# Optimization experiments

Measured on AMD Instinct MI355X. Metric: run time of the kernel, lower is better.

The kernel has to match this reference:

```python
import jax, jax.numpy as jnp
import numpy as np

VOC = 32000; D = 512; DFF = 2048; L = 4; H = 8; DH = D // H
NN = 256; K = 8; NB = 32; R = 128; SMAX = 1024; B = 4; S = 1024
STD = 0.02


def _ln(x, s, b):
    m = x.mean(-1, keepdims=True)
    v = ((x - m) ** 2).mean(-1, keepdims=True)
    return (x - m) / jnp.sqrt(v + 1e-5) * s + b


def setup_inputs() -> dict:
    key = jax.random.key(0)
    ks = jax.random.split(key, 24)
    p = {}
    p["input_ids"] = jax.random.randint(ks[0], (B, S), 0, VOC)
    p["token_emb"] = jax.random.normal(ks[1], (VOC, D)) * STD
    p["pos_emb"] = jax.random.normal(ks[2], (SMAX, D)) * STD
    # fixed shared basis buffers (orthogonalized at init in torch; random stand-in, same forward math)
    bA = jax.random.normal(ks[3], (NB, D, R))
    p["basis_A"] = bA / jnp.linalg.norm(bA.reshape(NB, -1), axis=-1)[:, None, None]
    be = jax.random.normal(ks[4], (NB, D))
    p["basis_emb"] = be / jnp.linalg.norm(be, axis=-1, keepdims=True)
    # per-layer params stacked on leading L axis; torch Linear weight is [out, in]
    p["q_w"] = jax.random.normal(ks[5], (L, D, D)) * STD
    p["q_b"] = jnp.zeros((L, D))
    p["k_w"] = jax.random.normal(ks[6], (L, D, D)) * STD
    p["k_b"] = jnp.zeros((L, D))
    p["ao_w"] = jax.random.normal(ks[7], (L, D, D)) * STD
    p["ao_b"] = jnp.zeros((L, D))
    p["recipe"] = jax.random.normal(ks[8], (L, NN, NB)) * 0.5
    p["ctx_pat"] = jax.random.normal(ks[9], (L, NN, H)) * 0.5
    p["vout_w"] = jax.random.normal(ks[10], (L, D, R)) * STD
    p["vout_b"] = jnp.zeros((L, D))
    p["up_w"] = jax.random.normal(ks[11], (L, DFF, D)) * STD
    p["up_b"] = jnp.zeros((L, DFF))
    p["down_w"] = jax.random.normal(ks[12], (L, D, DFF)) * STD
    p["down_b"] = jnp.zeros((L, D))
    p["ln1_s"] = jnp.ones((L, D)); p["ln1_b"] = jnp.zeros((L, D))
    p["ln2_s"] = jnp.ones((L, D)); p["ln2_b"] = jnp.zeros((L, D))
    p["lnf_s"] = jnp.ones((D,)); p["lnf_b"] = jnp.zeros((D,))
    return p


def reference(input_ids, token_emb, pos_emb, basis_A, basis_emb,
              q_w, q_b, k_w, k_b, ao_w, ao_b, recipe, ctx_pat,
              vout_w, vout_b, up_w, up_b, down_w, down_b,
              ln1_s, ln1_b, ln2_s, ln2_b, lnf_s, lnf_b):
    Bb, Ss = input_ids.shape
    x = token_emb[input_ids] + pos_emb[:Ss][None]  # [B,S,D]
    causal = jnp.tril(jnp.ones((Ss, Ss), dtype=bool))
    scale = 1.0 / np.sqrt(DH)
    for l in range(L):
        normed = _ln(x, ln1_s[l], ln1_b[l])
        Q = (normed @ q_w[l].T + q_b[l]).reshape(Bb, Ss, H, DH).transpose(0, 2, 1, 3)
        Kk = (normed @ k_w[l].T + k_b[l]).reshape(Bb, Ss, H, DH).transpose(0, 2, 1, 3)
        scores = jnp.einsum('bhsd,bhtd->bhst', Q, Kk) * scale
        scores = jnp.where(causal, scores, -jnp.inf)
        attn = jax.nn.softmax(scores, axis=-1)  # [B,H,S,S]
        # --- neuron-based dynamic V ---
        rec_sm = jax.nn.softmax(recipe[l], axis=-1)        # [NN,NB]
        emb_sem = rec_sm @ basis_emb                        # [NN,D]
        sem = normed @ emb_sem.T                            # [B,S,NN]
        summary = attn.mean(-1).transpose(0, 2, 1)          # [B,S,H]
        ctx = summary @ ctx_pat[l].T                        # [B,S,NN]
        fin = sem * jax.nn.sigmoid(ctx)
        topv, idx = jax.lax.top_k(fin, K)                   # [B,S,K]
        w = jax.nn.softmax(topv, axis=-1)
        sel = jax.nn.softmax(recipe[l][idx], axis=-1)       # [B,S,K,NB]
        token_recipe = jnp.einsum('bskn,bsk->bsn', sel, w)  # [B,S,NB]
        # reassociated contraction (same math as bsn,ndr->bsdr then bsd,bsdr->bsr)
        xA = jnp.einsum('bsd,ndr->bsnr', normed, basis_A)   # [B,S,NB,R]
        v_sem = jnp.einsum('bsn,bsnr->bsr', token_recipe, xA)
        Vv = (v_sem @ vout_w[l].T + vout_b[l]).reshape(Bb, Ss, H, DH).transpose(0, 2, 1, 3)
        ao = jnp.einsum('bhst,bhtd->bhsd', attn, Vv).transpose(0, 2, 1, 3).reshape(Bb, Ss, D)
        x = x + ao @ ao_w[l].T + ao_b[l]
        normed2 = _ln(x, ln2_s[l], ln2_b[l])
        h = jax.nn.gelu(normed2 @ up_w[l].T + up_b[l], approximate=False)
        x = x + h @ down_w[l].T + down_b[l]
    x = _ln(x, lnf_s, lnf_b)
    return x @ token_emb.T  # tied head, [B,S,vocab]
```

## Files before the change

### kernel.cpp

```cpp
#include <hip/hip_runtime.h>
#include <hip/hip_bf16.h>
#include <math.h>

typedef __attribute__((ext_vector_type(8))) short short8;
typedef __attribute__((ext_vector_type(4))) short short4v;
typedef __attribute__((ext_vector_type(8))) __bf16 bf16x8;
typedef __attribute__((ext_vector_type(4))) float f32x4;
typedef unsigned short ushort;
typedef unsigned int uint;

#define DEVI static __device__ __forceinline__

DEVI ushort f2bf(float f) {
  union { float f; unsigned u; } v; v.f = f;
  unsigned r = v.u + 0x7fffu + ((v.u >> 16) & 1u);
  return (ushort)(r >> 16);
}
DEVI float bf2f(ushort h) {
  union { unsigned u; float f; } v; v.u = (unsigned)h << 16; return v.f;
}
DEVI void gload16(const void* g, void* l) {
  __builtin_amdgcn_global_load_lds((const __attribute__((address_space(1))) void*)g,
                                   (__attribute__((address_space(3))) void*)l, 16, 0, 0);
}

DEVI void map_block(int gx, int gy, int BM, int bmode, int& n0, int& m0) {
  const int nwg = gx * gy;
  const int orig = blockIdx.y * gx + blockIdx.x;
  const int qq = nwg >> 3, rr = nwg & 7;
  const int xcd = orig & 7, sidx = orig >> 3;
  const int wg = (xcd < rr ? xcd * (qq + 1) : rr * (qq + 1) + (xcd - rr) * qq) + sidx;
  if (bmode == 0) {
    n0 = (wg % gx) * 128; m0 = (wg / gx) * BM;
  } else if (bmode > 0) {
    const int mh = bmode, bs = gx * mh;
    const int band = wg / bs, wi = wg - band * bs;
    n0 = (wi / mh) * 128;
    m0 = (band * mh + wi % mh) * BM;
  } else {
    const int bn = -bmode, gm = gy, bs = bn * gm;
    const int band = wg / bs, wi = wg - band * bs;
    m0 = (wi / bn) * BM;
    n0 = (band * bn + wi % bn) * 128;
  }
}

template<int BM, int EPI>
__global__ __launch_bounds__(256) void gemmT(
    const ushort* __restrict__ A, const ushort* __restrict__ B,
    void* __restrict__ Cv, const float* __restrict__ bias,
    int K, int lda, int ldb, int ldc, float scale, int bmode)
{
  constexpr int BK = 64;
  constexpr int MF = (BM + 31) / 32;
  constexpr int MH = BM / 2;
  constexpr int ACH = BM * BK / 2048;
  constexpr int BCH = 128 * BK / 2048;
  __shared__ ushort As[BM * BK];
  __shared__ ushort Bs[128 * BK];

  int n0, m0;
  map_block(gridDim.x, gridDim.y, BM, bmode, n0, m0);

  const int tid = threadIdx.x;
  const int lane = tid & 63, wv = tid >> 6;
  const int wm = wv >> 1, wn = wv & 1;
  const int l16 = lane & 15, lq = lane >> 4;

  f32x4 acc[MF][4];
#pragma unroll
  for (int i = 0; i < MF; i++)
#pragma unroll
    for (int j = 0; j < 4; j++) acc[i][j] = (f32x4){0.f, 0.f, 0.f, 0.f};

  const char* apS[ACH]; const char* bpS[BCH];
#pragma unroll
  for (int s = 0; s < ACH; s++) {
    int c = tid + 256 * s;
    apS[s] = (const char*)(A + (long)(m0 + (c >> 3)) * lda) + ((c & 7) << 4);
  }
#pragma unroll
  for (int s = 0; s < BCH; s++) {
    int c = tid + 256 * s;
    bpS[s] = (const char*)(B + (long)(n0 + (c >> 3)) * ldb) + ((c & 7) << 4);
  }

  for (int k0 = 0; k0 < K; k0 += BK) {
    const long kb = (long)k0 * 2;
#pragma unroll
    for (int s = 0; s < ACH; s++) gload16(apS[s] + kb, (char*)As + (tid + 256*s) * 16);
#pragma unroll
    for (int s = 0; s < BCH; s++) gload16(bpS[s] + kb, (char*)Bs + (tid + 256*s) * 16);
    __syncthreads();
#pragma unroll
    for (int ks = 0; ks < 2; ks++) {
      bf16x8 af[MF], bfr[4];
#pragma unroll
      for (int i = 0; i < MF; i++)
        af[i] = __builtin_bit_cast(bf16x8, *(const short8*)&As[(wm*MH + i*16 + l16)*BK + ks*32 + lq*8]);
#pragma unroll
      for (int j = 0; j < 4; j++)
        bfr[j] = __builtin_bit_cast(bf16x8, *(const short8*)&Bs[(wn*64 + j*16 + l16)*BK + ks*32 + lq*8]);
#pragma unroll
      for (int i = 0; i < MF; i++)
#pragma unroll
        for (int j = 0; j < 4; j++)
          acc[i][j] = __builtin_amdgcn_mfma_f32_16x16x32_bf16(af[i], bfr[j], acc[i][j], 0, 0, 0);
    }
    __syncthreads();
  }

  float* Cf = (float*)Cv;
  ushort* Ch = (ushort*)Cv;
#pragma unroll
  for (int i = 0; i < MF; i++) {
    const int row0 = m0 + wm*MH + i*16 + lq*4;
#pragma unroll
    for (int j = 0; j < 4; j++) {
      const int col = n0 + wn*64 + j*16 + l16;
      const float cb = bias ? bias[col] : 0.f;
#pragma unroll
      for (int t = 0; t < 4; t++) {
        float val = acc[i][j][t] * scale + cb;
        const long idx = (long)(row0 + t) * ldc + col;
        if (EPI == 1)      Ch[idx] = f2bf(val);
        else if (EPI == 2) { val = 0.5f * val * (1.f + erff(val * 0.70710678118654752f)); Ch[idx] = f2bf(val); }
        else if (EPI == 3) Cf[idx] += val;
        else               __builtin_nontemporal_store(val, Cf + idx);
      }
    }
  }
}

__global__ __launch_bounds__(256) void megag1(
    const ushort* __restrict__ A, const ushort* __restrict__ B,
    float* __restrict__ finb, ushort* __restrict__ qkh, ushort* __restrict__ XAb,
    const float* __restrict__ gate, const float* __restrict__ qkbias)
{
  constexpr int BK = 64;
  __shared__ ushort As[128 * BK];
  __shared__ ushort Bs[128 * BK];
  int n0, m0;
  map_block(gridDim.x, gridDim.y, 128, 8, n0, m0);

  const int tid = threadIdx.x;
  const int lane = tid & 63, wv = tid >> 6;
  const int wm = wv >> 1, wn = wv & 1;
  const int l16 = lane & 15, lq = lane >> 4;

  f32x4 acc[4][4];
#pragma unroll
  for (int i = 0; i < 4; i++)
#pragma unroll
    for (int j = 0; j < 4; j++) acc[i][j] = (f32x4){0.f, 0.f, 0.f, 0.f};

  const char* apS[4]; const char* bpS[4];
#pragma unroll
  for (int s = 0; s < 4; s++) {
    int c = tid + 256 * s;
    apS[s] = (const char*)(A + (long)(m0 + (c >> 3)) * 512) + ((c & 7) << 4);
    bpS[s] = (const char*)(B + (long)(n0 + (c >> 3)) * 512) + ((c & 7) << 4);
  }

  for (int k0 = 0; k0 < 512; k0 += BK) {
    const long kb = (long)k0 * 2;
#pragma unroll
    for (int s = 0; s < 4; s++) {
      gload16(apS[s] + kb, (char*)As + (tid + 256*s) * 16);
      gload16(bpS[s] + kb, (char*)Bs + (tid + 256*s) * 16);
    }
    __syncthreads();
#pragma unroll
    for (int ks = 0; ks < 2; ks++) {
      bf16x8 af[4], bfr[4];
#pragma unroll
      for (int i = 0; i < 4; i++) {
        af[i]  = __builtin_bit_cast(bf16x8, *(const short8*)&As[(wm*64 + i*16 + l16)*BK + ks*32 + lq*8]);
        bfr[i] = __builtin_bit_cast(bf16x8, *(const short8*)&Bs[(wn*64 + i*16 + l16)*BK + ks*32 + lq*8]);
      }
#pragma unroll
      for (int i = 0; i < 4; i++)
#pragma unroll
        for (int j = 0; j < 4; j++)
          acc[i][j] = __builtin_amdgcn_mfma_f32_16x16x32_bf16(af[i], bfr[j], acc[i][j], 0, 0, 0);
    }
    __syncthreads();
  }

#pragma unroll
  for (int i = 0; i < 4; i++) {
    const int row0 = m0 + wm*64 + i*16 + lq*4;
#pragma unroll
    for (int j = 0; j < 4; j++) {
      const int col = n0 + wn*64 + j*16 + l16;
      if (col < 256) {
        const float g = gate[col];
#pragma unroll
        for (int t = 0; t < 4; t++) finb[(long)(row0 + t) * 256 + col] = acc[i][j][t] * g;
      } else if (col < 1280) {
        const int c = col - 256;
        const float bb = qkbias[c];
#pragma unroll
        for (int t = 0; t < 4; t++) qkh[(long)(row0 + t) * 1024 + c] = f2bf(acc[i][j][t] + bb);
      } else {
        const int c = col - 1280;
#pragma unroll
        for (int t = 0; t < 4; t++) XAb[(long)(row0 + t) * 4096 + c] = f2bf(acc[i][j][t]);
      }
    }
  }
}

__global__ __launch_bounds__(256) void flash_kernel(
    const ushort* __restrict__ qk, const ushort* __restrict__ v,
    ushort* __restrict__ o)
{
  __shared__ ushort Ks[2][4096];
  __shared__ ushort VTs[2][4096];
  __shared__ ushort Ps[4096];
  const int qt = blockIdx.x, bh = blockIdx.y;
  const int b = bh >> 3, h = bh & 7;
  const int tid = threadIdx.x, lane = tid & 63, w = tid >> 6;
  const int l16 = lane & 15, lq = lane >> 4;
  const long tokbase = (long)b * 1024;
  const ushort* Qbase = qk + tokbase * 1024 + h * 64;
  const char*   Kbase = (const char*)(qk + tokbase * 1024 + 512 + h * 64);
  const ushort* Vbase = v + tokbase * 512 + h * 64;

  const int krow = tid >> 3, kcb = (tid & 7) << 4;
  const int vkv  = tid >> 2, vdb = (tid & 3) << 4;
  const int kswz = kcb ^ ((krow & 7) << 4);

  const int q0 = qt * 64;
  const int ntiles = qt + 1;

  const ushort* qrow = Qbase + (long)(q0 + w*16 + l16) * 1024;
  const bf16x8 qf0 = *(const bf16x8*)(qrow + lq*8);
  const bf16x8 qf1 = *(const bf16x8*)(qrow + 32 + lq*8);

  float m_[4] = {-1e30f, -1e30f, -1e30f, -1e30f};
  float l_[4] = {0.f, 0.f, 0.f, 0.f};
  f32x4 od[4];
#pragma unroll
  for (int dt = 0; dt < 4; dt++) od[dt] = (f32x4){0.f, 0.f, 0.f, 0.f};

  gload16(Kbase + (long)krow * 2048 + kswz, (char*)Ks[0] + tid * 16);
  gload16(Kbase + (long)(32 + krow) * 2048 + kswz, (char*)Ks[0] + 4096 + tid * 16);
  {
    const ushort* vr = Vbase + (long)vkv * 512 + vdb;
    short8 va = *(const short8*)vr;
    short8 vb = *(const short8*)(vr + 8);
#pragma unroll
    for (int j = 0; j < 8; j++) {
      int d1 = vdb + j, d2 = vdb + 8 + j;
      *(ushort*)((char*)VTs[0] + d1*128 + ((vkv*2) ^ ((d1 & 7) << 4))) = (ushort)va[j];
      *(ushort*)((char*)VTs[0] + d2*128 + ((vkv*2) ^ ((d2 & 7) << 4))) = (ushort)vb[j];
    }
  }
  __syncthreads();

  int cur = 0;
#pragma unroll 1
  for (int t = 0; t < ntiles; t++) {
    const bool hasn = (t + 1 < ntiles);
    short8 vaN, vbN;
    if (hasn) {
      const long n0g = (long)(t + 1) * 64;
      gload16(Kbase + (n0g + krow) * 2048 + kswz, (char*)Ks[cur ^ 1] + tid * 16);
      gload16(Kbase + (n0g + 32 + krow) * 2048 + kswz, (char*)Ks[cur ^ 1] + 4096 + tid * 16);
      const ushort* vr = Vbase + (n0g + vkv) * 512 + vdb;
      vaN = *(const short8*)vr;
      vbN = *(const short8*)(vr + 8);
    }

    f32x4 sa[4];
#pragma unroll
    for (int n = 0; n < 4; n++) sa[n] = (f32x4){0.f, 0.f, 0.f, 0.f};
#pragma unroll
    for (int ks = 0; ks < 2; ks++) {
      const bf16x8 qf = ks ? qf1 : qf0;
#pragma unroll
      for (int n = 0; n < 4; n++) {
        const int row = n*16 + l16;
        bf16x8 kf = *(const bf16x8*)((const char*)Ks[cur] + row*128 + ((ks*64 + lq*16) ^ ((row & 7) << 4)));
        sa[n] = __builtin_amdgcn_mfma_f32_16x16x32_bf16(qf, kf, sa[n], 0, 0, 0);
      }
    }

    const bool diag = (t == qt);
    float rowmax[4] = {-1e30f, -1e30f, -1e30f, -1e30f};
#pragma unroll
    for (int n = 0; n < 4; n++)
#pragma unroll
      for (int r = 0; r < 4; r++) {
        float sv = sa[n][r] * 0.125f;
        if (diag && (n*16 + l16 > w*16 + lq*4 + r)) sv = -1e30f;
        sa[n][r] = sv;
        rowmax[r] = fmaxf(rowmax[r], sv);
      }
#pragma unroll
    for (int r = 0; r < 4; r++)
#pragma unroll
      for (int off = 8; off; off >>= 1) rowmax[r] = fmaxf(rowmax[r], __shfl_xor(rowmax[r], off));

    float psum[4];
#pragma unroll
    for (int r = 0; r < 4; r++) {
      const float mn = fmaxf(m_[r], rowmax[r]);
      const float corr = __expf(m_[r] - mn);
      m_[r] = mn;
      l_[r] *= corr;
#pragma unroll
      for (int dt = 0; dt < 4; dt++) od[dt][r] *= corr;
      psum[r] = 0.f;
    }
#pragma unroll
    for (int n = 0; n < 4; n++)
#pragma unroll
      for (int r = 0; r < 4; r++) {
        const float pv = __expf(sa[n][r] - m_[r]);
        psum[r] += pv;
        const int prow = w*16 + lq*4 + r;
        *(ushort*)((char*)Ps + prow*128 + (((n*16 + l16)*2) ^ ((prow & 7) << 4))) = f2bf(pv);
      }
#pragma unroll
    for (int r = 0; r < 4; r++) {
#pragma unroll
      for (int off = 8; off; off >>= 1) psum[r] += __shfl_xor(psum[r], off);
      l_[r] += psum[r];
    }

#pragma unroll
    for (int ks = 0; ks < 2; ks++) {
      const int prow = w*16 + l16;
      bf16x8 pf = *(const bf16x8*)((const char*)Ps + prow*128 + ((ks*64 + lq*16) ^ ((prow & 7) << 4)));
#pragma unroll
      for (int dt = 0; dt < 4; dt++) {
        const int vrow = dt*16 + l16;
        bf16x8 vf = *(const bf16x8*)((const char*)VTs[cur] + vrow*128 + ((ks*64 + lq*16) ^ ((vrow & 7) << 4)));
        od[dt] = __builtin_amdgcn_mfma_f32_16x16x32_bf16(pf, vf, od[dt], 0, 0, 0);
      }
    }

    if (hasn) {
#pragma unroll
      for (int j = 0; j < 8; j++) {
        int d1 = vdb + j, d2 = vdb + 8 + j;
        *(ushort*)((char*)VTs[cur ^ 1] + d1*128 + ((vkv*2) ^ ((d1 & 7) << 4))) = (ushort)vaN[j];
        *(ushort*)((char*)VTs[cur ^ 1] + d2*128 + ((vkv*2) ^ ((d2 & 7) << 4))) = (ushort)vbN[j];
      }
    }
    __syncthreads();
    cur ^= 1;
  }

#pragma unroll
  for (int r = 0; r < 4; r++) {
    const float inv = 1.f / l_[r];
    ushort* orow = o + (tokbase + q0 + w*16 + lq*4 + r) * 512 + h * 64 + l16;
#pragma unroll
    for (int dt = 0; dt < 4; dt++) orow[dt*16] = f2bf(od[dt][r] * inv);
  }
}

DEVI void cvt8(const float* s, ushort* d) {
  float4 u = *(const float4*)s, v = *(const float4*)(s + 4);
  short8 o;
  o[0]=(short)f2bf(u.x); o[1]=(short)f2bf(u.y); o[2]=(short)f2bf(u.z); o[3]=(short)f2bf(u.w);
  o[4]=(short)f2bf(v.x); o[5]=(short)f2bf(v.y); o[6]=(short)f2bf(v.z); o[7]=(short)f2bf(v.w);
  *(short8*)d = o;
}
__global__ __launch_bounds__(256) void cvt_all(
    const float* __restrict__ q_w, const float* __restrict__ k_w,
    const float* __restrict__ ao_w, const float* __restrict__ vout_w,
    const float* __restrict__ up_w, const float* __restrict__ down_w,
    const float* __restrict__ temb, const float* __restrict__ q_b,
    const float* __restrict__ k_b,
    ushort* __restrict__ Bcat, ushort* __restrict__ aowh, ushort* __restrict__ voutwh,
    ushort* __restrict__ upwh, ushort* __restrict__ downwh, ushort* __restrict__ tembh,
    float* __restrict__ qkb)
{
  long u = (long)blockIdx.x * 256 + threadIdx.x;
  if (u < 262144) {
    long e = u * 8;
    int l = (int)(e >> 19);
    long rem = e & 524287;
    bool isk = rem >= 262144;
    long so = rem & 262143;
    cvt8((isk ? k_w : q_w) + (long)l * 262144 + so,
         Bcat + (long)l * 2752512 + 131072 + (isk ? 262144 : 0) + so);
    return;
  }
  u -= 262144;
  if (u < 131072) { cvt8(ao_w + u*8, aowh + u*8); return; }
  u -= 131072;
  if (u < 32768)  { cvt8(vout_w + u*8, voutwh + u*8); return; }
  u -= 32768;
  if (u < 524288) { cvt8(up_w + u*8, upwh + u*8); return; }
  u -= 524288;
  if (u < 524288) { cvt8(down_w + u*8, downwh + u*8); return; }
  u -= 524288;
  if (u < 2048000){ cvt8(temb + u*8, tembh + u*8); return; }
  u -= 2048000;
  {
    long i8 = u * 8;
    int l = (int)(i8 >> 10), c = (int)(i8 & 1023);
    const float* src = (c < 512) ? (q_b + l*512 + c) : (k_b + l*512 + c - 512);
    float* dst = qkb + i8;
    *(float4*)dst = *(const float4*)src;
    *(float4*)(dst + 4) = *(const float4*)(src + 4);
  }
}

__global__ __launch_bounds__(256) void transpose_basisA(
    const float* __restrict__ src, ushort* __restrict__ Bcat)
{
  __shared__ ushort tile[64][132];
  const int n = blockIdx.x;
  const int d0 = blockIdx.y * 64;
  const int l = blockIdx.z;
  ushort* dst = Bcat + (long)l * 2752512 + 655360;
  const int tid = threadIdx.x;
#pragma unroll
  for (int it = 0; it < 8; it++) {
    int d = it * 8 + (tid >> 5);
    int rr = (tid & 31) * 4;
    float4 v = *(const float4*)(src + ((long)n * 512 + d0 + d) * 128 + rr);
    tile[d][rr + 0] = f2bf(v.x);
    tile[d][rr + 1] = f2bf(v.y);
    tile[d][rr + 2] = f2bf(v.z);
    tile[d][rr + 3] = f2bf(v.w);
  }
  __syncthreads();
#pragma unroll
  for (int it = 0; it < 4; it++) {
    int rr = it * 32 + (tid >> 3);
    int dof = (tid & 7) * 8;
    short8 s;
#pragma unroll
    for (int j = 0; j < 8; j++) s[j] = (short)tile[dof + j][rr];
    *(short8*)(dst + ((long)n * 128 + rr) * 512 + d0 + dof) = s;
  }
}

__global__ __launch_bounds__(256) void embed_ln(
    const int* __restrict__ ids, const float* __restrict__ tok,
    const float* __restrict__ pos, const float* __restrict__ gam,
    const float* __restrict__ bet, float* __restrict__ x, ushort* __restrict__ outh)
{
  int row = blockIdx.x * 4 + (threadIdx.x >> 6);
  int lane = threadIdx.x & 63;
  int id = ids[row], sp = row & 1023;
  const float* tp = tok + (long)id * 512;
  const float* pp = pos + (long)sp * 512;
  float4 v0 = *(const float4*)(tp + lane*4);
  float4 p0 = *(const float4*)(pp + lane*4);
  float4 v1 = *(const float4*)(tp + 256 + lane*4);
  float4 p1 = *(const float4*)(pp + 256 + lane*4);
  v0.x+=p0.x; v0.y+=p0.y; v0.z+=p0.z; v0.w+=p0.w;
  v1.x+=p1.x; v1.y+=p1.y; v1.z+=p1.z; v1.w+=p1.w;
  *(float4*)(x + (long)row*512 + lane*4) = v0;
  *(float4*)(x + (long)row*512 + 256 + lane*4) = v1;
  float s = v0.x+v0.y+v0.z+v0.w + v1.x+v1.y+v1.z+v1.w;
#pragma unroll
  for (int o = 32; o; o >>= 1) s += __shfl_xor(s, o);
  float mean = s * (1.f/512.f);
  float d0=v0.x-mean, d1=v0.y-mean, d2=v0.z-mean, d3=v0.w-mean;
  float e0=v1.x-mean, e1=v1.y-mean, e2=v1.z-mean, e3=v1.w-mean;
  float qv = d0*d0+d1*d1+d2*d2+d3*d3 + e0*e0+e1*e1+e2*e2+e3*e3;
#pragma unroll
  for (int o = 32; o; o >>= 1) qv += __shfl_xor(qv, o);
  float inv = rsqrtf(qv * (1.f/512.f) + 1e-5f);
  float4 g0 = *(const float4*)(gam + lane*4);
  float4 g1 = *(const float4*)(gam + 256 + lane*4);
  float4 b0 = *(const float4*)(bet + lane*4);
  float4 b1 = *(const float4*)(bet + 256 + lane*4);
  short4v o0, o1;
  o0[0]=(short)f2bf(d0*inv*g0.x + b0.x); o0[1]=(short)f2bf(d1*inv*g0.y + b0.y);
  o0[2]=(short)f2bf(d2*inv*g0.z + b0.z); o0[3]=(short)f2bf(d3*inv*g0.w + b0.w);
  o1[0]=(short)f2bf(e0*inv*g1.x + b1.x); o1[1]=(short)f2bf(e1*inv*g1.y + b1.y);
  o1[2]=(short)f2bf(e2*inv*g1.z + b1.z); o1[3]=(short)f2bf(e3*inv*g1.w + b1.w);
  *(short4v*)(outh + (long)row*512 + lane*4) = o0;
  *(short4v*)(outh + (long)row*512 + 256 + lane*4) = o1;
}

__global__ __launch_bounds__(256) void ln_kernel(
    const float* __restrict__ in, ushort* __restrict__ outh,
    const float* __restrict__ gam, const float* __restrict__ bet)
{
  int row = blockIdx.x * 4 + (threadIdx.x >> 6);
  int lane = threadIdx.x & 63;
  const float* p = in + (long)row * 512;
  float4 v0 = *(const float4*)(p + lane * 4);
  float4 v1 = *(const float4*)(p + 256 + lane * 4);
  float s = v0.x+v0.y+v0.z+v0.w + v1.x+v1.y+v1.z+v1.w;
#pragma unroll
  for (int o = 32; o; o >>= 1) s += __shfl_xor(s, o);
  float mean = s * (1.f/512.f);
  float d0=v0.x-mean, d1=v0.y-mean, d2=v0.z-mean, d3=v0.w-mean;
  float e0=v1.x-mean, e1=v1.y-mean, e2=v1.z-mean, e3=v1.w-mean;
  float qv = d0*d0+d1*d1+d2*d2+d3*d3 + e0*e0+e1*e1+e2*e2+e3*e3;
#pragma unroll
  for (int o = 32; o; o >>= 1) qv += __shfl_xor(qv, o);
  float inv = rsqrtf(qv * (1.f/512.f) + 1e-5f);
  float4 g0 = *(const float4*)(gam + lane*4);
  float4 g1 = *(const float4*)(gam + 256 + lane*4);
  float4 b0 = *(const float4*)(bet + lane*4);
  float4 b1 = *(const float4*)(bet + 256 + lane*4);
  short4v o0, o1;
  o0[0]=(short)f2bf(d0*inv*g0.x + b0.x); o0[1]=(short)f2bf(d1*inv*g0.y + b0.y);
  o0[2]=(short)f2bf(d2*inv*g0.z + b0.z); o0[3]=(short)f2bf(d3*inv*g0.w + b0.w);
  o1[0]=(short)f2bf(e0*inv*g1.x + b1.x); o1[1]=(short)f2bf(e1*inv*g1.y + b1.y);
  o1[2]=(short)f2bf(e2*inv*g1.z + b1.z); o1[3]=(short)f2bf(e3*inv*g1.w + b1.w);
  *(short4v*)(outh + (long)row*512 + lane*4) = o0;
  *(short4v*)(outh + (long)row*512 + 256 + lane*4) = o1;
}

__global__ __launch_bounds__(64) void precompute_kernel(
    const float* __restrict__ recipe, const float* __restrict__ basis_emb,
    const float* __restrict__ ctx_pat, float* __restrict__ rec_sm,
    ushort* __restrict__ Bcat, float* __restrict__ gate)
{
  int ln = blockIdx.x;
  int l = ln >> 8, n = ln & 255;
  int lane = threadIdx.x;
  const float* r = recipe + (long)ln * 32;
  float rv[32];
  float m = -1e30f;
#pragma unroll
  for (int j = 0; j < 32; j++) { rv[j] = r[j]; m = fmaxf(m, rv[j]); }
  float sum = 0.f;
#pragma unroll
  for (int j = 0; j < 32; j++) { rv[j] = expf(rv[j] - m); sum += rv[j]; }
  float inv = 1.f / sum;
#pragma unroll
  for (int j = 0; j < 32; j++) rv[j] *= inv;
  if (lane < 32) rec_sm[(long)ln * 32 + lane] = rv[lane];
  ushort* dst = Bcat + (long)l * 2752512 + (long)n * 512;
#pragma unroll
  for (int cc = 0; cc < 8; cc++) {
    int c = lane + cc * 64;
    float acc = 0.f;
#pragma unroll
    for (int j = 0; j < 32; j++) acc += rv[j] * basis_emb[j * 512 + c];
    dst[c] = f2bf(acc);
  }
  if (lane == 0) {
    float sh = 0.f;
#pragma unroll
    for (int h = 0; h < 8; h++) sh += ctx_pat[(long)ln * 8 + h];
    gate[ln] = 1.f / (1.f + expf(-sh * (1.f/1024.f)));
  }
}

__global__ __launch_bounds__(256) void topkvsem_kernel(
    const float* __restrict__ fin, const float* __restrict__ rec_sm_l,
    const ushort* __restrict__ XA, ushort* __restrict__ out)
{
  __shared__ float trs[4][32];
  int wv = threadIdx.x >> 6, lane = threadIdx.x & 63;
  int t = blockIdx.x * 4 + wv;
  const float* f = fin + (long)t * 256;
  float v0 = f[lane], v1 = f[lane+64], v2 = f[lane+128], v3 = f[lane+192];
  int i0 = lane, i1 = lane+64, i2 = lane+128, i3 = lane+192;
  float topv[8]; int topi[8];
#pragma unroll
  for (int it = 0; it < 8; it++) {
    float bm = v0; int bi = i0;
    if (v1 > bm || (v1 == bm && i1 < bi)) { bm = v1; bi = i1; }
    if (v2 > bm || (v2 == bm && i2 < bi)) { bm = v2; bi = i2; }
    if (v3 > bm || (v3 == bm && i3 < bi)) { bm = v3; bi = i3; }
#pragma unroll
    for (int o = 32; o; o >>= 1) {
      float om = __shfl_xor(bm, o);
      int oi = __shfl_xor(bi, o);
      if (om > bm || (om == bm && oi < bi)) { bm = om; bi = oi; }
    }
    topv[it] = bm; topi[it] = bi;
    if (i0 == bi) v0 = -1e30f;
    if (i1 == bi) v1 = -1e30f;
    if (i2 == bi) v2 = -1e30f;
    if (i3 == bi) v3 = -1e30f;
  }
  float w[8], wsum = 0.f;
#pragma unroll
  for (int k = 0; k < 8; k++) { w[k] = expf(topv[k] - topv[0]); wsum += w[k]; }
  float winv = 1.f / wsum;
  if (lane < 32) {
    float acc = 0.f;
#pragma unroll
    for (int k = 0; k < 8; k++)
      acc += (w[k] * winv) * rec_sm_l[(long)topi[k] * 32 + lane];
    trs[wv][lane] = acc;
  }
  __syncthreads();
  const ushort* xa = XA + (long)t * 4096;
  float a0 = 0.f, a1 = 0.f;
#pragma unroll
  for (int n = 0; n < 32; n++) {
    float wn = trs[wv][n];
    uint u = *(const uint*)&xa[n*128 + 2*lane];
    a0 += wn * bf2f((ushort)(u & 0xffffu));
    a1 += wn * bf2f((ushort)(u >> 16));
  }
  uint o = (uint)f2bf(a0) | ((uint)f2bf(a1) << 16);
  *(uint*)&out[(long)t * 128 + 2*lane] = o;
}

extern "C" void kernel_launch(void* const* d_in, const int* in_sizes, int n_in,
                              void* d_out, int out_size, void* d_ws, size_t ws_size,
                              hipStream_t stream) {
  (void)in_sizes; (void)n_in; (void)out_size; (void)ws_size;
  const int*   ids       = (const int*)  d_in[0];
  const float* token_emb = (const float*)d_in[1];
  const float* pos_emb   = (const float*)d_in[2];
  const float* basis_A   = (const float*)d_in[3];
  const float* basis_emb = (const float*)d_in[4];
  const float* q_w  = (const float*)d_in[5];
  const float* q_b  = (const float*)d_in[6];
  const float* k_w  = (const float*)d_in[7];
  const float* k_b  = (const float*)d_in[8];
  const float* ao_w = (const float*)d_in[9];
  const float* ao_b = (const float*)d_in[10];
  const float* recipe  = (const float*)d_in[11];
  const float* ctx_pat = (const float*)d_in[12];
  const float* vout_w  = (const float*)d_in[13];
  const float* vout_b  = (const float*)d_in[14];
  const float* up_w    = (const float*)d_in[15];
  const float* up_b    = (const float*)d_in[16];
  const float* down_w  = (const float*)d_in[17];
  const float* down_b  = (const float*)d_in[18];
  const float* ln1_s = (const float*)d_in[19];
  const float* ln1_b = (const float*)d_in[20];
  const float* ln2_s = (const float*)d_in[21];
  const float* ln2_b = (const float*)d_in[22];
  const float* lnf_s = (const float*)d_in[23];
  const float* lnf_b = (const float*)d_in[24];
  float* out = (float*)d_out;

  float* ws    = (float*)d_ws;
  float* x     = ws;
  float* finb  = x + 2097152;
  float* recsm = finb + 1048576;
  float* gate  = recsm + 32768;
  float* qkb   = gate + 1024;
  ushort* u = (ushort*)(qkb + 4096);
  ushort* nrmh    = u; u += 2097152;
  ushort* vsemh   = u; u += 524288;
  ushort* Bcat    = u; u += 11010048;
  ushort* aowh    = u; u += 1048576;
  ushort* voutwh  = u; u += 262144;
  ushort* upwh    = u; u += 4194304;
  ushort* downwh  = u; u += 4194304;
  ushort* tembh   = u; u += 16384000;

  ushort* XAb = (ushort*)out;
  ushort* HF  = (ushort*)out;
  ushort* qkh = (ushort*)out + 16777216;
  ushort* vvh = (ushort*)out + 20971520;
  ushort* aoh = (ushort*)out + 23068672;

  cvt_all<<<13762, 256, 0, stream>>>(q_w, k_w, ao_w, vout_w, up_w, down_w,
      token_emb, q_b, k_b, Bcat, aowh, voutwh, upwh, downwh, tembh, qkb);
  transpose_basisA<<<dim3(32, 8, 4), 256, 0, stream>>>(basis_A, Bcat);
  precompute_kernel<<<1024, 64, 0, stream>>>(recipe, basis_emb, ctx_pat, recsm, Bcat, gate);
  embed_ln<<<1024, 256, 0, stream>>>(ids, token_emb, pos_emb, ln1_s, ln1_b, x, nrmh);

  for (int l = 0; l < 4; l++) {
    if (l) ln_kernel<<<1024, 256, 0, stream>>>(x, nrmh, ln1_s + l*512, ln1_b + l*512);
    megag1<<<dim3(42, 32), 256, 0, stream>>>(nrmh, Bcat + (long)l*2752512,
        finb, qkh, XAb, gate + l*256, qkb + l*1024);
    topkvsem_kernel<<<1024, 256, 0, stream>>>(finb, recsm + (long)l*8192, XAb, vsemh);
    gemmT<32,1><<<dim3(4, 128), 256, 0, stream>>>(vsemh, voutwh + (long)l*65536, vvh,
        vout_b + l*512, 128, 128, 128, 512, 1.f, 32);
    flash_kernel<<<dim3(16, 32), 256, 0, stream>>>(qkh, vvh, aoh);
    gemmT<32,3><<<dim3(4, 128), 256, 0, stream>>>(aoh, aowh + (long)l*262144, x,
        ao_b + l*512, 512, 512, 512, 512, 1.f, 32);
    ln_kernel<<<1024, 256, 0, stream>>>(x, nrmh, ln2_s + l*512, ln2_b + l*512);
    gemmT<64,2><<<dim3(16, 64), 256, 0, stream>>>(nrmh, upwh + (long)l*1048576, (void*)HF,
        up_b + l*2048, 512, 512, 512, 2048, 1.f, 16);
    gemmT<32,3><<<dim3(4, 128), 256, 0, stream>>>(HF, downwh + (long)l*1048576, x,
        down_b + l*512, 2048, 2048, 2048, 512, 1.f, 32);
  }

  ln_kernel<<<1024, 256, 0, stream>>>(x, nrmh, lnf_s, lnf_b);
  gemmT<128,4><<<dim3(250, 32), 256, 0, stream>>>(nrmh, tembh, out, nullptr,
      512, 512, 512, 32000, 1.f, -25);
}
```

Measured before the change: 1.069 ms.

## Pair causal flash query tiles per block and stage fp32 GEMM epilogue via LDS

The flash attention kernel now processes two query tiles per block, tile p and tile 15-p. Every block then does the same number of KV tiles, which balances causal work across a half-sized grid. Separately, the fp32 GEMM epilogues (residual accumulate and logits store) are staged through a shared-memory tile so each thread writes contiguous 16-byte vectors instead of scattered scalar stores. The cost is fewer flash blocks, with less latency hiding per CU, plus extra LDS and barriers in the GEMM epilogue.

```diff
diff --git a/kernel.cpp b/kernel.cpp
--- a/kernel.cpp
+++ b/kernel.cpp
@@ -58,6 +58,7 @@
   constexpr int BCH = 128 * BK / 2048;
   __shared__ ushort As[BM * BK];
   __shared__ ushort Bs[128 * BK];
+  __shared__ float Cs[(EPI == 3 || EPI == 4) ? MH * 132 : 1];
 
   int n0, m0;
   map_block(gridDim.x, gridDim.y, BM, bmode, n0, m0);
@@ -112,21 +113,56 @@
 
   float* Cf = (float*)Cv;
   ushort* Ch = (ushort*)Cv;
-#pragma unroll
-  for (int i = 0; i < MF; i++) {
-    const int row0 = m0 + wm*MH + i*16 + lq*4;
-#pragma unroll
-    for (int j = 0; j < 4; j++) {
-      const int col = n0 + wn*64 + j*16 + l16;
-      const float cb = bias ? bias[col] : 0.f;
-#pragma unroll
-      for (int t = 0; t < 4; t++) {
-        float val = acc[i][j][t] * scale + cb;
-        const long idx = (long)(row0 + t) * ldc + col;
-        if (EPI == 1)      Ch[idx] = f2bf(val);
-        else if (EPI == 2) { val = 0.5f * val * (1.f + erff(val * 0.70710678118654752f)); Ch[idx] = f2bf(val); }
-        else if (EPI == 3) Cf[idx] += val;
-        else               __builtin_nontemporal_store(val, Cf + idx);
+
+  if (EPI == 3 || EPI == 4) {
+    constexpr int TPR = 256 / MH;
+    constexpr int CPT = 128 / TPR;
+    const int r2 = tid / TPR, c0 = (tid % TPR) * CPT;
+#pragma unroll
+    for (int half = 0; half < 2; half++) {
+      __syncthreads();
+      if (wm == half) {
+#pragma unroll
+        for (int i = 0; i < MF; i++)
+#pragma unroll
+          for (int j = 0; j < 4; j++) {
+            const int col = wn*64 + j*16 + l16;
+            const float cb = bias ? bias[n0 + col] : 0.f;
+#pragma unroll
+            for (int t = 0; t < 4; t++)
+              Cs[(i*16 + lq*4 + t)*132 + col] = acc[i][j][t] * scale + cb;
+          }
+      }
+      __syncthreads();
+      float* dst = Cf + (long)(m0 + half*MH + r2) * ldc + n0 + c0;
+      const float* src = &Cs[r2 * 132 + c0];
+#pragma unroll
+      for (int q = 0; q < CPT/4; q++) {
+        f32x4 v = ((const f32x4*)src)[q];
+        if (EPI == 3) {
+          f32x4 o = ((f32x4*)dst)[q];
+          v += o;
+          ((f32x4*)dst)[q] = v;
+        } else {
+          __builtin_nontemporal_store(v, (f32x4*)dst + q);
+        }
+      }
+    }
+  } else {
+#pragma unroll
+    for (int i = 0; i < MF; i++) {
+      const int row0 = m0 + wm*MH + i*16 + lq*4;
+#pragma unroll
+      for (int j = 0; j < 4; j++) {
+        const int col = n0 + wn*64 + j*16 + l16;
+        const float cb = bias ? bias[col] : 0.f;
+#pragma unroll
+        for (int t = 0; t < 4; t++) {
+          float val = acc[i][j][t] * scale + cb;
+          const long idx = (long)(row0 + t) * ldc + col;
+          if (EPI == 1)      Ch[idx] = f2bf(val);
+          else               { val = 0.5f * val * (1.f + erff(val * 0.70710678118654752f)); Ch[idx] = f2bf(val); }
+        }
       }
     }
   }
@@ -218,7 +254,7 @@
   __shared__ ushort Ks[2][4096];
   __shared__ ushort VTs[2][4096];
   __shared__ ushort Ps[4096];
-  const int qt = blockIdx.x, bh = blockIdx.y;
+  const int p = blockIdx.x, bh = blockIdx.y;
   const int b = bh >> 3, h = bh & 7;
   const int tid = threadIdx.x, lane = tid & 63, w = tid >> 6;
   const int l16 = lane & 15, lq = lane >> 4;
@@ -231,135 +267,139 @@
   const int vkv  = tid >> 2, vdb = (tid & 3) << 4;
   const int kswz = kcb ^ ((krow & 7) << 4);
 
-  const int q0 = qt * 64;
-  const int ntiles = qt + 1;
-
-  const ushort* qrow = Qbase + (long)(q0 + w*16 + l16) * 1024;
-  const bf16x8 qf0 = *(const bf16x8*)(qrow + lq*8);
-  const bf16x8 qf1 = *(const bf16x8*)(qrow + 32 + lq*8);
-
-  float m_[4] = {-1e30f, -1e30f, -1e30f, -1e30f};
-  float l_[4] = {0.f, 0.f, 0.f, 0.f};
-  f32x4 od[4];
-#pragma unroll
-  for (int dt = 0; dt < 4; dt++) od[dt] = (f32x4){0.f, 0.f, 0.f, 0.f};
-
-  gload16(Kbase + (long)krow * 2048 + kswz, (char*)Ks[0] + tid * 16);
-  gload16(Kbase + (long)(32 + krow) * 2048 + kswz, (char*)Ks[0] + 4096 + tid * 16);
-  {
-    const ushort* vr = Vbase + (long)vkv * 512 + vdb;
-    short8 va = *(const short8*)vr;
-    short8 vb = *(const short8*)(vr + 8);
-#pragma unroll
-    for (int j = 0; j < 8; j++) {
-      int d1 = vdb + j, d2 = vdb + 8 + j;
-      *(ushort*)((char*)VTs[0] + d1*128 + ((vkv*2) ^ ((d1 & 7) << 4))) = (ushort)va[j];
-      *(ushort*)((char*)VTs[0] + d2*128 + ((vkv*2) ^ ((d2 & 7) << 4))) = (ushort)vb[j];
-    }
-  }
-  __syncthreads();
-
-  int cur = 0;
 #pragma unroll 1
-  for (int t = 0; t < ntiles; t++) {
-    const bool hasn = (t + 1 < ntiles);
-    short8 vaN, vbN;
-    if (hasn) {
-      const long n0g = (long)(t + 1) * 64;
-      gload16(Kbase + (n0g + krow) * 2048 + kswz, (char*)Ks[cur ^ 1] + tid * 16);
-      gload16(Kbase + (n0g + 32 + krow) * 2048 + kswz, (char*)Ks[cur ^ 1] + 4096 + tid * 16);
-      const ushort* vr = Vbase + (n0g + vkv) * 512 + vdb;
-      vaN = *(const short8*)vr;
-      vbN = *(const short8*)(vr + 8);
-    }
-
-    f32x4 sa[4];
-#pragma unroll
-    for (int n = 0; n < 4; n++) sa[n] = (f32x4){0.f, 0.f, 0.f, 0.f};
-#pragma unroll
-    for (int ks = 0; ks < 2; ks++) {
-      const bf16x8 qf = ks ? qf1 : qf0;
-#pragma unroll
-      for (int n = 0; n < 4; n++) {
-        const int row = n*16 + l16;
-        bf16x8 kf = *(const bf16x8*)((const char*)Ks[cur] + row*128 + ((ks*64 + lq*16) ^ ((row & 7) << 4)));
-        sa[n] = __builtin_amdgcn_mfma_f32_16x16x32_bf16(qf, kf, sa[n], 0, 0, 0);
-      }
-    }
-
-    const bool diag = (t == qt);
-    float rowmax[4] = {-1e30f, -1e30f, -1e30f, -1e30f};
-#pragma unroll
-    for (int n = 0; n < 4; n++)
-#pragma unroll
-      for (int r = 0; r < 4; r++) {
-        float sv = sa[n][r] * 0.125f;
-        if (diag && (n*16 + l16 > w*16 + lq*4 + r)) sv = -1e30f;
-        sa[n][r] = sv;
-        rowmax[r] = fmaxf(rowmax[r], sv);
-      }
-#pragma unroll
-    for (int r = 0; r < 4; r++)
-#pragma unroll
-      for (int off = 8; off; off >>= 1) rowmax[r] = fmaxf(rowmax[r], __shfl_xor(rowmax[r], off));
-
-    float psum[4];
-#pragma unroll
-    for (int r = 0; r < 4; r++) {
-      const float mn = fmaxf(m_[r], rowmax[r]);
-      const float corr = __expf(m_[r] - mn);
-      m_[r] = mn;
-      l_[r] *= corr;
-#pragma unroll
-      for (int dt = 0; dt < 4; dt++) od[dt][r] *= corr;
-      psum[r] = 0.f;
-    }
-#pragma unroll
-    for (int n = 0; n < 4; n++)
-#pragma unroll
-      for (int r = 0; r < 4; r++) {
-        const float pv = __expf(sa[n][r] - m_[r]);
-        psum[r] += pv;
-        const int prow = w*16 + lq*4 + r;
-        *(ushort*)((char*)Ps + prow*128 + (((n*16 + l16)*2) ^ ((prow & 7) << 4))) = f2bf(pv);
-      }
-#pragma unroll
-    for (int r = 0; r < 4; r++) {
-#pragma unroll
-      for (int off = 8; off; off >>= 1) psum[r] += __shfl_xor(psum[r], off);
-      l_[r] += psum[r];
-    }
-
-#pragma unroll
-    for (int ks = 0; ks < 2; ks++) {
-      const int prow = w*16 + l16;
-      bf16x8 pf = *(const bf16x8*)((const char*)Ps + prow*128 + ((ks*64 + lq*16) ^ ((prow & 7) << 4)));
-#pragma unroll
-      for (int dt = 0; dt < 4; dt++) {
-        const int vrow = dt*16 + l16;
-        bf16x8 vf = *(const bf16x8*)((const char*)VTs[cur] + vrow*128 + ((ks*64 + lq*16) ^ ((vrow & 7) << 4)));
-        od[dt] = __builtin_amdgcn_mfma_f32_16x16x32_bf16(pf, vf, od[dt], 0, 0, 0);
-      }
-    }
-
-    if (hasn) {
+  for (int half = 0; half < 2; half++) {
+    const int qt = half ? (15 - p) : p;
+    const int q0 = qt * 64;
+    const int ntiles = qt + 1;
+
+    const ushort* qrow = Qbase + (long)(q0 + w*16 + l16) * 1024;
+    const bf16x8 qf0 = *(const bf16x8*)(qrow + lq*8);
+    const bf16x8 qf1 = *(const bf16x8*)(qrow + 32 + lq*8);
+
+    float m_[4] = {-1e30f, -1e30f, -1e30f, -1e30f};
+    float l_[4] = {0.f, 0.f, 0.f, 0.f};
+    f32x4 od[4];
+#pragma unroll
+    for (int dt = 0; dt < 4; dt++) od[dt] = (f32x4){0.f, 0.f, 0.f, 0.f};
+
+    gload16(Kbase + (long)krow * 2048 + kswz, (char*)Ks[0] + tid * 16);
+    gload16(Kbase + (long)(32 + krow) * 2048 + kswz, (char*)Ks[0] + 4096 + tid * 16);
+    {
+      const ushort* vr = Vbase + (long)vkv * 512 + vdb;
+      short8 va = *(const short8*)vr;
+      short8 vb = *(const short8*)(vr + 8);
 #pragma unroll
       for (int j = 0; j < 8; j++) {
         int d1 = vdb + j, d2 = vdb + 8 + j;
-        *(ushort*)((char*)VTs[cur ^ 1] + d1*128 + ((vkv*2) ^ ((d1 & 7) << 4))) = (ushort)vaN[j];
-        *(ushort*)((char*)VTs[cur ^ 1] + d2*128 + ((vkv*2) ^ ((d2 & 7) << 4))) = (ushort)vbN[j];
+        *(ushort*)((char*)VTs[0] + d1*128 + ((vkv*2) ^ ((d1 & 7) << 4))) = (ushort)va[j];
+        *(ushort*)((char*)VTs[0] + d2*128 + ((vkv*2) ^ ((d2 & 7) << 4))) = (ushort)vb[j];
       }
     }
     __syncthreads();
-    cur ^= 1;
-  }
-
-#pragma unroll
-  for (int r = 0; r < 4; r++) {
-    const float inv = 1.f / l_[r];
-    ushort* orow = o + (tokbase + q0 + w*16 + lq*4 + r) * 512 + h * 64 + l16;
-#pragma unroll
-    for (int dt = 0; dt < 4; dt++) orow[dt*16] = f2bf(od[dt][r] * inv);
+
+    int cur = 0;
+#pragma unroll 1
+    for (int t = 0; t < ntiles; t++) {
+      const bool hasn = (t + 1 < ntiles);
+      short8 vaN, vbN;
+      if (hasn) {
+        const long n0g = (long)(t + 1) * 64;
+        gload16(Kbase + (n0g + krow) * 2048 + kswz, (char*)Ks[cur ^ 1] + tid * 16);
+        gload16(Kbase + (n0g + 32 + krow) * 2048 + kswz, (char*)Ks[cur ^ 1] + 4096 + tid * 16);
+        const ushort* vr = Vbase + (n0g + vkv) * 512 + vdb;
+        vaN = *(const short8*)vr;
+        vbN = *(const short8*)(vr + 8);
+      }
+
+      f32x4 sa[4];
+#pragma unroll
+      for (int n = 0; n < 4; n++) sa[n] = (f32x4){0.f, 0.f, 0.f, 0.f};
+#pragma unroll
+      for (int ks = 0; ks < 2; ks++) {
+        const bf16x8 qf = ks ? qf1 : qf0;
+#pragma unroll
+        for (int n = 0; n < 4; n++) {
+          const int row = n*16 + l16;
+          bf16x8 kf = *(const bf16x8*)((const char*)Ks[cur] + row*128 + ((ks*64 + lq*16) ^ ((row & 7) << 4)));
+          sa[n] = __builtin_amdgcn_mfma_f32_16x16x32_bf16(qf, kf, sa[n], 0, 0, 0);
+        }
+      }
+
+      const bool diag = (t == qt);
+      float rowmax[4] = {-1e30f, -1e30f, -1e30f, -1e30f};
+#pragma unroll
+      for (int n = 0; n < 4; n++)
+#pragma unroll
+        for (int r = 0; r < 4; r++) {
+          float sv = sa[n][r] * 0.125f;
+          if (diag && (n*16 + l16 > w*16 + lq*4 + r)) sv = -1e30f;
+          sa[n][r] = sv;
+          rowmax[r] = fmaxf(rowmax[r], sv);
+        }
+#pragma unroll
+      for (int r = 0; r < 4; r++)
+#pragma unroll
+        for (int off = 8; off; off >>= 1) rowmax[r] = fmaxf(rowmax[r], __shfl_xor(rowmax[r], off));
+
+      float psum[4];
+#pragma unroll
+      for (int r = 0; r < 4; r++) {
+        const float mn = fmaxf(m_[r], rowmax[r]);
+        const float corr = __expf(m_[r] - mn);
+        m_[r] = mn;
+        l_[r] *= corr;
+#pragma unroll
+        for (int dt = 0; dt < 4; dt++) od[dt][r] *= corr;
+        psum[r] = 0.f;
+      }
+#pragma unroll
+      for (int n = 0; n < 4; n++)
+#pragma unroll
+        for (int r = 0; r < 4; r++) {
+          const float pv = __expf(sa[n][r] - m_[r]);
+          psum[r] += pv;
+          const int prow = w*16 + lq*4 + r;
+          *(ushort*)((char*)Ps + prow*128 + (((n*16 + l16)*2) ^ ((prow & 7) << 4))) = f2bf(pv);
+        }
+#pragma unroll
+      for (int r = 0; r < 4; r++) {
+#pragma unroll
+        for (int off = 8; off; off >>= 1) psum[r] += __shfl_xor(psum[r], off);
+        l_[r] += psum[r];
+      }
+
+#pragma unroll
+      for (int ks = 0; ks < 2; ks++) {
+        const int prow = w*16 + l16;
+        bf16x8 pf = *(const bf16x8*)((const char*)Ps + prow*128 + ((ks*64 + lq*16) ^ ((prow & 7) << 4)));
+#pragma unroll
+        for (int dt = 0; dt < 4; dt++) {
+          const int vrow = dt*16 + l16;
+          bf16x8 vf = *(const bf16x8*)((const char*)VTs[cur] + vrow*128 + ((ks*64 + lq*16) ^ ((vrow & 7) << 4)));
+          od[dt] = __builtin_amdgcn_mfma_f32_16x16x32_bf16(pf, vf, od[dt], 0, 0, 0);
+        }
+      }
+
+      if (hasn) {
+#pragma unroll
+        for (int j = 0; j < 8; j++) {
+          int d1 = vdb + j, d2 = vdb + 8 + j;
+          *(ushort*)((char*)VTs[cur ^ 1] + d1*128 + ((vkv*2) ^ ((d1 & 7) << 4))) = (ushort)vaN[j];
+          *(ushort*)((char*)VTs[cur ^ 1] + d2*128 + ((vkv*2) ^ ((d2 & 7) << 4))) = (ushort)vbN[j];
+        }
+      }
+      __syncthreads();
+      cur ^= 1;
+    }
+
+#pragma unroll
+    for (int r = 0; r < 4; r++) {
+      const float inv = 1.f / l_[r];
+      ushort* orow = o + (tokbase + q0 + w*16 + lq*4 + r) * 512 + h * 64 + l16;
+#pragma unroll
+      for (int dt = 0; dt < 4; dt++) orow[dt*16] = f2bf(od[dt][r] * inv);
+    }
   }
 }
 
@@ -673,7 +713,7 @@
     topkvsem_kernel<<<1024, 256, 0, stream>>>(finb, recsm + (long)l*8192, XAb, vsemh);
     gemmT<32,1><<<dim3(4, 128), 256, 0, stream>>>(vsemh, voutwh + (long)l*65536, vvh,
         vout_b + l*512, 128, 128, 128, 512, 1.f, 32);
-    flash_kernel<<<dim3(16, 32), 256, 0, stream>>>(qkh, vvh, aoh);
+    flash_kernel<<<dim3(8, 32), 256, 0, stream>>>(qkh, vvh, aoh);
     gemmT<32,3><<<dim3(4, 128), 256, 0, stream>>>(aoh, aowh + (long)l*262144, x,
         ao_b + l*512, 512, 512, 512, 512, 1.f, 32);
     ln_kernel<<<1024, 256, 0, stream>>>(x, nrmh, ln2_s + l*512, ln2_b + l*512);
```

Measured after the change: 2.468 ms. 2.31x slower.
